# Kernel optimization log

Measured on AMD Instinct MI355X. Metric: run time of the kernel, lower is better.

## Reference

```python
import jax, jax.numpy as jnp
import numpy as np

N_ITER = 30
NMF_EPS = 1e-20
IP_EPS = 1e-20


def nmf_update(Tn, Vn, Yn, eps=NMF_EPS):
    # Tn: (I,K), Vn: (K,J), Yn: (I,J) complex
    Rn = Tn @ Vn
    magR = jnp.abs(Rn)
    YdR = jnp.abs(Yn) ** 2 / (magR ** 2 + eps)   # (I,J)
    Rd = 1.0 / (magR + eps)
    Tn_new = Tn * jnp.sqrt((YdR @ Vn.T) / (Rd @ Vn.T + eps))
    Rn2 = Tn_new @ Vn
    Rd2 = 1.0 / (jnp.abs(Rn2) + eps)
    Vn_new = Vn * jnp.sqrt((Tn_new.T @ YdR) / (Tn_new.T @ Rd2 + eps))
    return Tn_new, Vn_new, Tn_new @ Vn_new


def _ilrma(X, T0, V0):
    M, J, I, _ = X.shape
    N = M
    Xp = jnp.transpose(X, (2, 0, 1, 3))                     # (I,M,J,2)
    X_c = (Xp[..., 0] + 1j * Xp[..., 1]).astype(jnp.complex64)  # (I,M,J)
    eye_M = jnp.eye(M, dtype=jnp.complex64)
    W0 = jnp.tile(eye_M[None], (I, 1, 1))                   # (I,N,M)

    def body(carry, _):
        W, T, V = carry
        Y = jnp.einsum('inm,imj->inj', W, X_c)              # (I,N,J)
        for n in range(N):  # small fixed loop over sources
            Tn, Vn, Rn = nmf_update(T[:, :, n], V[:, :, n], Y[:, n, :])
            T = T.at[:, :, n].set(Tn)
            V = V.at[:, :, n].set(Vn)
            inv_Rn = 1.0 / (Rn + IP_EPS)                    # (I,J) real
            Xw = X_c * jnp.sqrt(inv_Rn)[:, None, :]         # (I,M,J)
            D = jnp.matmul(Xw, jnp.conj(jnp.swapaxes(Xw, 1, 2))) / J  # (I,M,M)
            D_reg = D + IP_EPS * eye_M[None]
            A = jnp.matmul(W, D_reg)                        # (I,N,M)
            e_n = jnp.broadcast_to(eye_M[:, n][None, :, None], (I, M, 1))
            b = jnp.linalg.solve(A, e_n)                    # (I,M,1)
            bH = jnp.conj(jnp.swapaxes(b, 1, 2))
            denom = jnp.matmul(jnp.matmul(bH, D_reg), b).real
            denom = jnp.sqrt(denom + IP_EPS)                # (I,1,1)
            w = jnp.conj((b / denom)[:, :, 0])              # (I,M)
            W = W.at[:, n, :].set(w)
        return (W, T, V), None

    (W, T, V), _ = jax.lax.scan(body, (W0, T0, V0), None, length=N_ITER)
    Y = jnp.einsum('inm,imj->inj', W, X_c)                  # (I,N,J)
    Yo = jnp.transpose(Y, (1, 2, 0))                        # (N,J,I)
    return jnp.stack([Yo.real, Yo.imag], axis=-1)           # (N,J,I,2)


def setup_inputs() -> dict:
    key = jax.random.key(0)
    k1, k2, k3 = jax.random.split(key, 3)
    M, J, I, K = 2, 3000, 2049, 8
    X = jax.random.normal(k1, (M, J, I, 2), dtype=jnp.float32)
    T_init = jax.random.uniform(k2, (I, K, M), dtype=jnp.float32) * (1 - 1e-8) + 1e-8
    V_init = jax.random.uniform(k3, (K, J, M), dtype=jnp.float32) * (1 - 1e-8) + 1e-8
    return {"X": X, "T_init": T_init, "V_init": V_init}


def reference(X, T_init, V_init):
    return _ilrma(X, T_init, V_init)
```

## Files before the change

kernel.cpp:

```cpp
#include <hip/hip_runtime.h>

#define DEVINL __device__ __forceinline__

constexpr int J_ = 3000;
constexpr int I_ = 2049;
constexpr int K_ = 8;
constexpr int NITER = 30;
constexpr float EPS = 1e-20f;
constexpr int JH = 1500;
constexpr int JHP = 1536;
constexpr int JP = 2 * JHP;
constexpr int NL = JHP / 256;
constexpr int TJB = 256;
constexpr int NJTP = JHP / TJB;

typedef float f32x2 __attribute__((ext_vector_type(2)));

DEVINL float waveRed(float v) {
#pragma unroll
  for (int off = 32; off > 0; off >>= 1) v += __shfl_xor(v, off, 64);
  return v;
}

DEVINL float frcp(float x) { return __builtin_amdgcn_rcpf(x); }
DEVINL f32x2 sp(float s) { return (f32x2){s, s}; }
DEVINL f32x2 xy(float4 v) { return (f32x2){v.x, v.y}; }
DEVINL f32x2 zw(float4 v) { return (f32x2){v.z, v.w}; }

__global__ void k_init(const float* __restrict__ Tin, const float* __restrict__ Vin,
                       float* __restrict__ T, float2* __restrict__ V2, float2* __restrict__ W2) {
  int idx = blockIdx.x * 256 + threadIdx.x;
  if (idx < I_ * K_ * 2) {
    int n = idx & 1, rem = idx >> 1;
    int k = rem & 7, i = rem >> 3;
    T[n * I_ * K_ + i * K_ + k] = Tin[idx];
  }
  if (idx < K_ * JP) {
    int k = idx / JP, j = idx - k * JP;
    float2 v = (j < J_) ? ((const float2*)Vin)[k * J_ + j] : make_float2(0.f, 0.f);
    V2[k * JP + j] = v;
  }
  if (idx < I_) {
    W2[idx * 4 + 0] = make_float2(1.f, 0.f);
    W2[idx * 4 + 1] = make_float2(0.f, 0.f);
    W2[idx * 4 + 2] = make_float2(0.f, 0.f);
    W2[idx * 4 + 3] = make_float2(1.f, 0.f);
  }
}

__global__ __launch_bounds__(256) void k_transpose(const float2* __restrict__ X, float2* __restrict__ Xt) {
  __shared__ float2 tile[32][33];
  int m = blockIdx.z;
  int i0 = blockIdx.x * 32, j0 = blockIdx.y * 32;
  int tx = threadIdx.x & 31, ty = threadIdx.x >> 5;
  for (int r = ty; r < 32; r += 8) {
    int j = j0 + r, i = i0 + tx;
    tile[r][tx] = (i < I_ && j < J_) ? X[((size_t)m * J_ + j) * I_ + i] : make_float2(0.f, 0.f);
  }
  __syncthreads();
  for (int r = ty; r < 32; r += 8) {
    int i = i0 + r, j = j0 + tx;
    if (i < I_) Xt[((size_t)m * I_ + i) * JP + j] = tile[tx][r];
  }
}

template <bool DO_C, bool DO_A>
__global__ __launch_bounds__(256, 4) void k_CA(const float4* __restrict__ Xt4,
                                               float2* __restrict__ W2,
                                               float* __restrict__ T,
                                               const float4* __restrict__ V4,
                                               float2* __restrict__ YdR2) {
  const int i = blockIdx.x, t = threadIdx.x;
  const int wave = t >> 6, lane = t & 63;
  f32x2 Tp[K_];
#pragma unroll
  for (int k = 0; k < K_; k++) {
    Tp[k] = (f32x2){T[i * K_ + k], T[I_ * K_ + i * K_ + k]};
  }
  const float4* x0r = Xt4 + (size_t)i * JHP;
  const float4* x1r = Xt4 + (size_t)(I_ + i) * JHP;

  __shared__ f32x2 sR[2][NL][256];
  __shared__ float sred[4][32];
  __shared__ float sout[32];
  __shared__ float sbc[8];

  if constexpr (DO_C) {
    f32x2 an00 = sp(0.f), an11 = sp(0.f), acre = sp(0.f), acim = sp(0.f);
#pragma unroll 2
    for (int l = 0; l < NL; l++) {
      int j2 = t + l * 256;
      float4 x0 = x0r[j2], x1 = x1r[j2];
      f32x2 rA = sp(0.f), rB = sp(0.f);
#pragma unroll
      for (int k = 0; k < K_; k++) {
        float4 vp = V4[(size_t)k * JHP + j2];
        rA += Tp[k] * xy(vp);
        rB += Tp[k] * zw(vp);
      }
      if constexpr (DO_A) {
        sR[0][l][t] = rA;
        sR[1][l][t] = rB;
      }
      f32x2 iA = (f32x2){frcp(rA.x + EPS), frcp(rA.y + EPS)};
      f32x2 iB = (f32x2){frcp(rB.x + EPS), frcp(rB.y + EPS)};
      float n00a = x0.x * x0.x + x0.y * x0.y, n00b = x0.z * x0.z + x0.w * x0.w;
      float n11a = x1.x * x1.x + x1.y * x1.y, n11b = x1.z * x1.z + x1.w * x1.w;
      float crea = x0.x * x1.x + x0.y * x1.y, creb = x0.z * x1.z + x0.w * x1.w;
      float cima = x0.y * x1.x - x0.x * x1.y, cimb = x0.w * x1.z - x0.z * x1.w;
      an00 += sp(n00a) * iA + sp(n00b) * iB;
      an11 += sp(n11a) * iA + sp(n11b) * iB;
      acre += sp(crea) * iA + sp(creb) * iB;
      acim += sp(cima) * iA + sp(cimb) * iB;
    }
    float vals[8] = {an00.x, an11.x, acre.x, acim.x, an00.y, an11.y, acre.y, acim.y};
#pragma unroll
    for (int q = 0; q < 8; q++) {
      float v = waveRed(vals[q]);
      if (lane == 0) sred[wave][q] = v;
    }
    __syncthreads();
    if (t < 8) sout[t] = sred[0][t] + sred[1][t] + sred[2][t] + sred[3][t];
    __syncthreads();
    if (t == 0) {
      const double Jinv = 1.0 / (double)J_;
      double D[2][4];
#pragma unroll
      for (int s2 = 0; s2 < 2; s2++) {
        D[s2][0] = (double)sout[s2 * 4 + 0] * Jinv + (double)EPS;
        D[s2][1] = (double)sout[s2 * 4 + 1] * Jinv + (double)EPS;
        D[s2][2] = (double)sout[s2 * 4 + 2] * Jinv;
        D[s2][3] = (double)sout[s2 * 4 + 3] * Jinv;
      }
      double Wd[2][2][2];
#pragma unroll
      for (int r = 0; r < 2; r++)
#pragma unroll
        for (int c = 0; c < 2; c++) {
          float2 w = W2[i * 4 + r * 2 + c];
          Wd[r][c][0] = w.x;
          Wd[r][c][1] = w.y;
        }
      for (int n2 = 0; n2 < 2; n2++) {
        double d00 = D[n2][0], d11 = D[n2][1], dre = D[n2][2], dim = D[n2][3];
        double A[2][2][2];
#pragma unroll
        for (int r = 0; r < 2; r++) {
          A[r][0][0] = Wd[r][0][0] * d00 + (Wd[r][1][0] * dre + Wd[r][1][1] * dim);
          A[r][0][1] = Wd[r][0][1] * d00 + (Wd[r][1][1] * dre - Wd[r][1][0] * dim);
          A[r][1][0] = Wd[r][1][0] * d11 + (Wd[r][0][0] * dre - Wd[r][0][1] * dim);
          A[r][1][1] = Wd[r][1][1] * d11 + (Wd[r][0][1] * dre + Wd[r][0][0] * dim);
        }
        double detre = A[0][0][0] * A[1][1][0] - A[0][0][1] * A[1][1][1]
                     - (A[0][1][0] * A[1][0][0] - A[0][1][1] * A[1][0][1]);
        double detim = A[0][0][0] * A[1][1][1] + A[0][0][1] * A[1][1][0]
                     - (A[0][1][0] * A[1][0][1] + A[0][1][1] * A[1][0][0]);
        double b0re, b0im, b1re, b1im;
        if (n2 == 0) { b0re = A[1][1][0]; b0im = A[1][1][1]; b1re = -A[1][0][0]; b1im = -A[1][0][1]; }
        else         { b0re = -A[0][1][0]; b0im = -A[0][1][1]; b1re = A[0][0][0]; b1im = A[0][0][1]; }
        double dmag = detre * detre + detim * detim;
        double t0re = (b0re * detre + b0im * detim) / dmag, t0im = (b0im * detre - b0re * detim) / dmag;
        double t1re = (b1re * detre + b1im * detim) / dmag, t1im = (b1im * detre - b1re * detim) / dmag;
        double pre = t0re * t1re + t0im * t1im, pim = t0re * t1im - t0im * t1re;
        double quad = d00 * (t0re * t0re + t0im * t0im) + d11 * (t1re * t1re + t1im * t1im)
                    + 2.0 * (dre * pre - dim * pim);
        double denom = sqrt(quad + (double)EPS);
        double w0re = t0re / denom, w0im = -t0im / denom;
        double w1re = t1re / denom, w1im = -t1im / denom;
        Wd[n2][0][0] = w0re; Wd[n2][0][1] = w0im;
        Wd[n2][1][0] = w1re; Wd[n2][1][1] = w1im;
        W2[i * 4 + n2 * 2 + 0] = make_float2((float)w0re, (float)w0im);
        W2[i * 4 + n2 * 2 + 1] = make_float2((float)w1re, (float)w1im);
      }
      if (DO_A) {
        sbc[0] = (float)(Wd[0][0][0] * Wd[0][0][0] + Wd[0][0][1] * Wd[0][0][1]);
        sbc[1] = (float)(Wd[0][1][0] * Wd[0][1][0] + Wd[0][1][1] * Wd[0][1][1]);
        sbc[2] = (float)(2.0 * (Wd[0][0][0] * Wd[0][1][0] + Wd[0][0][1] * Wd[0][1][1]));
        sbc[3] = (float)(-2.0 * (Wd[0][0][1] * Wd[0][1][0] - Wd[0][0][0] * Wd[0][1][1]));
        sbc[4] = (float)(Wd[1][0][0] * Wd[1][0][0] + Wd[1][0][1] * Wd[1][0][1]);
        sbc[5] = (float)(Wd[1][1][0] * Wd[1][1][0] + Wd[1][1][1] * Wd[1][1][1]);
        sbc[6] = (float)(2.0 * (Wd[1][0][0] * Wd[1][1][0] + Wd[1][0][1] * Wd[1][1][1]));
        sbc[7] = (float)(-2.0 * (Wd[1][0][1] * Wd[1][1][0] - Wd[1][0][0] * Wd[1][1][1]));
      }
    }
  } else {
    if (t == 0) {
      float2 w00 = W2[i * 4 + 0], w01 = W2[i * 4 + 1], w10 = W2[i * 4 + 2], w11 = W2[i * 4 + 3];
      sbc[0] = w00.x * w00.x + w00.y * w00.y;
      sbc[1] = w01.x * w01.x + w01.y * w01.y;
      sbc[2] = 2.f * (w00.x * w01.x + w00.y * w01.y);
      sbc[3] = -2.f * (w00.y * w01.x - w00.x * w01.y);
      sbc[4] = w10.x * w10.x + w10.y * w10.y;
      sbc[5] = w11.x * w11.x + w11.y * w11.y;
      sbc[6] = 2.f * (w10.x * w11.x + w10.y * w11.y);
      sbc[7] = -2.f * (w10.y * w11.x - w10.x * w11.y);
    }
  }

  if constexpr (DO_A) {
    __syncthreads();
    const f32x2 alp = (f32x2){sbc[0], sbc[4]}, btp = (f32x2){sbc[1], sbc[5]};
    const f32x2 gmp = (f32x2){sbc[2], sbc[6]}, dlp = (f32x2){sbc[3], sbc[7]};
    f32x2 nT[K_], dT[K_];
#pragma unroll
    for (int k = 0; k < K_; k++) { nT[k] = sp(0.f); dT[k] = sp(0.f); }
    float2* y0r = YdR2 + (size_t)i * JHP;
    float2* y1r = YdR2 + (size_t)(I_ + i) * JHP;
#pragma unroll 1
    for (int l = 0; l < NL; l++) {
      int j2 = t + l * 256;
      float4 x0 = x0r[j2], x1 = x1r[j2];
      f32x2 rA, rB;
      if constexpr (DO_C) {
        rA = sR[0][l][t];
        rB = sR[1][l][t];
      } else {
        rA = sp(0.f); rB = sp(0.f);
#pragma unroll
        for (int k = 0; k < K_; k++) {
          float4 vp = V4[(size_t)k * JHP + j2];
          rA += Tp[k] * xy(vp);
          rB += Tp[k] * zw(vp);
        }
      }
      float n00a = x0.x * x0.x + x0.y * x0.y, n00b = x0.z * x0.z + x0.w * x0.w;
      float n11a = x1.x * x1.x + x1.y * x1.y, n11b = x1.z * x1.z + x1.w * x1.w;
      float crea = x0.x * x1.x + x0.y * x1.y, creb = x0.z * x1.z + x0.w * x1.w;
      float cima = x0.y * x1.x - x0.x * x1.y, cimb = x0.w * x1.z - x0.z * x1.w;
      f32x2 aA = alp * n00a + btp * n11a + gmp * crea + dlp * cima;
      f32x2 aB = alp * n00b + btp * n11b + gmp * creb + dlp * cimb;
      f32x2 ydrA = aA * (f32x2){frcp(rA.x * rA.x + EPS), frcp(rA.y * rA.y + EPS)};
      f32x2 ydrB = aB * (f32x2){frcp(rB.x * rB.x + EPS), frcp(rB.y * rB.y + EPS)};
      f32x2 rdA = (f32x2){frcp(rA.x + EPS), frcp(rA.y + EPS)};
      f32x2 rdB = (f32x2){frcp(rB.x + EPS), frcp(rB.y + EPS)};
      y0r[j2] = make_float2(ydrA.x, ydrB.x);
      y1r[j2] = make_float2(ydrA.y, ydrB.y);
#pragma unroll
      for (int k = 0; k < K_; k++) {
        float4 vp = V4[(size_t)k * JHP + j2];
        nT[k] += ydrA * xy(vp) + ydrB * zw(vp);
        dT[k] += rdA * xy(vp) + rdB * zw(vp);
      }
    }
#pragma unroll
    for (int k = 0; k < K_; k++) {
      float a = waveRed(nT[k].x); if (lane == 0) sred[wave][k] = a;
      float b = waveRed(dT[k].x); if (lane == 0) sred[wave][8 + k] = b;
      float c = waveRed(nT[k].y); if (lane == 0) sred[wave][16 + k] = c;
      float d = waveRed(dT[k].y); if (lane == 0) sred[wave][24 + k] = d;
    }
    __syncthreads();
    if (t < 32) sout[t] = sred[0][t] + sred[1][t] + sred[2][t] + sred[3][t];
    __syncthreads();
    if (t < 16) {
      int n = t >> 3, k = t & 7;
      float num = sout[n * 16 + k];
      float den = sout[n * 16 + 8 + k];
      float told = T[n * I_ * K_ + i * K_ + k];
      T[n * I_ * K_ + i * K_ + k] = told * sqrtf(num / (den + EPS));
    }
  }
}

__global__ __launch_bounds__(TJB, 4) void k_passB(const float* __restrict__ T,
                                                  const float4* __restrict__ V4,
                                                  const float2* __restrict__ YdR2,
                                                  float2* __restrict__ partial2, int iseg) {
  int t = threadIdx.x;
  int jt = blockIdx.x, s = blockIdx.y, n = blockIdx.z;
  int j2 = jt * TJB + t;
  f32x2 va2[K_];
#pragma unroll
  for (int k = 0; k < K_; k++) {
    float4 vp = V4[(size_t)k * JHP + j2];
    va2[k] = (n == 0) ? (f32x2){vp.x, vp.z} : (f32x2){vp.y, vp.w};
  }
  int i0 = s * iseg, i1 = min(i0 + iseg, I_);
  const float2* yb = YdR2 + (size_t)n * I_ * JHP;
  const float* Tb = T + (size_t)n * I_ * K_;
  f32x2 nV[K_], dV[K_];
#pragma unroll
  for (int k = 0; k < K_; k++) { nV[k] = sp(0.f); dV[k] = sp(0.f); }
#pragma unroll 4
  for (int i = i0; i < i1; i++) {
    const float4* tp = (const float4*)(Tb + i * K_);
    float4 t03 = tp[0], t47 = tp[1];
    float Tn[K_] = {t03.x, t03.y, t03.z, t03.w, t47.x, t47.y, t47.z, t47.w};
    float2 yl = yb[(size_t)i * JHP + j2];
    f32x2 y = (f32x2){yl.x, yl.y};
    f32x2 R = sp(0.f);
#pragma unroll
    for (int k = 0; k < K_; k++) R += sp(Tn[k]) * va2[k];
    f32x2 rd = (f32x2){frcp(R.x + EPS), frcp(R.y + EPS)};
#pragma unroll
    for (int k = 0; k < K_; k++) {
      nV[k] += sp(Tn[k]) * y;
      dV[k] += sp(Tn[k]) * rd;
    }
  }
  if (j2 < JH) {
    size_t b0 = (size_t)((s * 2 + n) * 2 + 0) * K_ * JH;
    size_t b1 = (size_t)((s * 2 + n) * 2 + 1) * K_ * JH;
#pragma unroll
    for (int k = 0; k < K_; k++) {
      partial2[b0 + (size_t)k * JH + j2] = make_float2(nV[k].x, nV[k].y);
      partial2[b1 + (size_t)k * JH + j2] = make_float2(dV[k].x, dV[k].y);
    }
  }
}

__global__ void k_finV(const float* __restrict__ partial, float* __restrict__ Vf, int nseg) {
  int idx = blockIdx.x * 256 + threadIdx.x;
  if (idx >= 2 * K_ * J_) return;
  int n = idx / (K_ * J_);
  int rem = idx - n * (K_ * J_);
  int k = rem / J_, j = rem - k * J_;
  float num = 0.f, den = 0.f;
  for (int s = 0; s < nseg; s++) {
    num += partial[((size_t)((s * 2 + n) * 2 + 0) * K_ + k) * J_ + j];
    den += partial[((size_t)((s * 2 + n) * 2 + 1) * K_ + k) * J_ + j];
  }
  float res = sqrtf(num / (den + EPS));
  Vf[((size_t)k * JP + j) * 2 + n] *= res;
}

__global__ __launch_bounds__(256) void k_output(const float2* __restrict__ Xt,
                                                const float2* __restrict__ W2,
                                                float2* __restrict__ out) {
  __shared__ float2 tile[2][32][33];
  int i0 = blockIdx.x * 32, j0 = blockIdx.y * 32;
  int tx = threadIdx.x & 31, ty = threadIdx.x >> 5;
  for (int r = ty; r < 32; r += 8) {
    int i = i0 + r, j = j0 + tx;
    if (i < I_ && j < J_) {
      float2 w00 = W2[i * 4 + 0], w01 = W2[i * 4 + 1], w10 = W2[i * 4 + 2], w11 = W2[i * 4 + 3];
      float2 x0 = Xt[(size_t)i * JP + j], x1 = Xt[((size_t)I_ + i) * JP + j];
      tile[0][r][tx] = make_float2(w00.x * x0.x - w00.y * x0.y + w01.x * x1.x - w01.y * x1.y,
                                   w00.x * x0.y + w00.y * x0.x + w01.x * x1.y + w01.y * x1.x);
      tile[1][r][tx] = make_float2(w10.x * x0.x - w10.y * x0.y + w11.x * x1.x - w11.y * x1.y,
                                   w10.x * x0.y + w10.y * x0.x + w11.x * x1.y + w11.y * x1.x);
    }
  }
  __syncthreads();
  for (int r = ty; r < 32; r += 8) {
    int j = j0 + r, i = i0 + tx;
    if (i < I_ && j < J_) {
      out[((size_t)0 * J_ + j) * I_ + i] = tile[0][tx][r];
      out[((size_t)1 * J_ + j) * I_ + i] = tile[1][tx][r];
    }
  }
}

extern "C" void kernel_launch(void* const* d_in, const int* in_sizes, int n_in,
                              void* d_out, int out_size, void* d_ws, size_t ws_size,
                              hipStream_t stream) {
  const float* X = (const float*)d_in[0];
  const float* Tin = (const float*)d_in[1];
  const float* Vin = (const float*)d_in[2];

  char* ws = (char*)d_ws;
  size_t off = 0;
  auto alloc = [&](size_t bytes) {
    void* p = ws + off;
    off = (off + bytes + 255) & ~(size_t)255;
    return p;
  };
  float2* Xt = (float2*)alloc((size_t)2 * I_ * JP * sizeof(float2));
  float2* YdR2 = (float2*)alloc((size_t)2 * I_ * JHP * sizeof(float2));
  float2* V2 = (float2*)alloc((size_t)K_ * JP * sizeof(float2));
  float* T = (float*)alloc((size_t)2 * I_ * K_ * sizeof(float));
  float2* W2 = (float2*)alloc((size_t)I_ * 4 * sizeof(float2));
  size_t per_seg = (size_t)2 * 2 * K_ * J_ * sizeof(float);
  int nseg = (off + 64 * per_seg <= ws_size) ? 64 : ((off + 32 * per_seg <= ws_size) ? 32 : 16);
  float* partial = (float*)alloc((size_t)nseg * per_seg);
  int iseg = (I_ + nseg - 1) / nseg;
  (void)in_sizes; (void)n_in; (void)out_size;

  const float4* Xt4 = (const float4*)Xt;
  const float4* V4 = (const float4*)V2;

  k_init<<<(I_ * K_ * 2 + 255) / 256, 256, 0, stream>>>(Tin, Vin, T, V2, W2);
  dim3 tg((I_ + 31) / 32, JP / 32, 2);
  k_transpose<<<tg, 256, 0, stream>>>((const float2*)X, Xt);

  k_CA<false, true><<<I_, 256, 0, stream>>>(Xt4, W2, T, V4, YdR2);
  for (int it = 0; it < NITER; it++) {
    k_passB<<<dim3(NJTP, nseg, 2), TJB, 0, stream>>>(T, V4, YdR2, (float2*)partial, iseg);
    k_finV<<<(2 * K_ * J_ + 255) / 256, 256, 0, stream>>>(partial, (float*)V2, nseg);
    if (it < NITER - 1) {
      k_CA<true, true><<<I_, 256, 0, stream>>>(Xt4, W2, T, V4, YdR2);
    } else {
      k_CA<true, false><<<I_, 256, 0, stream>>>(Xt4, W2, T, V4, YdR2);
    }
  }
  dim3 og((I_ + 31) / 32, (J_ + 31) / 32);
  k_output<<<og, 256, 0, stream>>>(Xt, W2, (float2*)d_out);
}
```

Before: 3.196 ms.

## Process two frequency rows per block in k_CA to share V loads

Each k_CA block now handles rows i and i+1025, so the grid shrinks to 1025 blocks. In the covariance pass the V tile loaded per j is reused for both rows' model reconstructions. The IP solve is factored into a helper run by two threads, and the T-update pass loops over both rows. Shared memory for sR doubles and register pressure rises, which may reduce occupancy. The second pass still reloads V separately for each row.

```diff
diff --git a/kernel.cpp b/kernel.cpp
--- a/kernel.cpp
+++ b/kernel.cpp
@@ -13,6 +13,7 @@
 constexpr int NL = JHP / 256;
 constexpr int TJB = 256;
 constexpr int NJTP = JHP / TJB;
+constexpr int IBLK = 1025;
 
 typedef float f32x2 __attribute__((ext_vector_type(2)));
 
@@ -64,200 +65,243 @@
   }
 }
 
+DEVINL void ip_solve(const float* sout8, float2* W2, int irow, float* sbc8, bool fill_sbc) {
+  const double Jinv = 1.0 / (double)J_;
+  double D[2][4];
+#pragma unroll
+  for (int s2 = 0; s2 < 2; s2++) {
+    D[s2][0] = (double)sout8[s2 * 4 + 0] * Jinv + (double)EPS;
+    D[s2][1] = (double)sout8[s2 * 4 + 1] * Jinv + (double)EPS;
+    D[s2][2] = (double)sout8[s2 * 4 + 2] * Jinv;
+    D[s2][3] = (double)sout8[s2 * 4 + 3] * Jinv;
+  }
+  double Wd[2][2][2];
+#pragma unroll
+  for (int r = 0; r < 2; r++)
+#pragma unroll
+    for (int c = 0; c < 2; c++) {
+      float2 w = W2[irow * 4 + r * 2 + c];
+      Wd[r][c][0] = w.x;
+      Wd[r][c][1] = w.y;
+    }
+  for (int n2 = 0; n2 < 2; n2++) {
+    double d00 = D[n2][0], d11 = D[n2][1], dre = D[n2][2], dim = D[n2][3];
+    double A[2][2][2];
+#pragma unroll
+    for (int r = 0; r < 2; r++) {
+      A[r][0][0] = Wd[r][0][0] * d00 + (Wd[r][1][0] * dre + Wd[r][1][1] * dim);
+      A[r][0][1] = Wd[r][0][1] * d00 + (Wd[r][1][1] * dre - Wd[r][1][0] * dim);
+      A[r][1][0] = Wd[r][1][0] * d11 + (Wd[r][0][0] * dre - Wd[r][0][1] * dim);
+      A[r][1][1] = Wd[r][1][1] * d11 + (Wd[r][0][1] * dre + Wd[r][0][0] * dim);
+    }
+    double detre = A[0][0][0] * A[1][1][0] - A[0][0][1] * A[1][1][1]
+                 - (A[0][1][0] * A[1][0][0] - A[0][1][1] * A[1][0][1]);
+    double detim = A[0][0][0] * A[1][1][1] + A[0][0][1] * A[1][1][0]
+                 - (A[0][1][0] * A[1][0][1] + A[0][1][1] * A[1][0][0]);
+    double b0re, b0im, b1re, b1im;
+    if (n2 == 0) { b0re = A[1][1][0]; b0im = A[1][1][1]; b1re = -A[1][0][0]; b1im = -A[1][0][1]; }
+    else         { b0re = -A[0][1][0]; b0im = -A[0][1][1]; b1re = A[0][0][0]; b1im = A[0][0][1]; }
+    double dmag = detre * detre + detim * detim;
+    double t0re = (b0re * detre + b0im * detim) / dmag, t0im = (b0im * detre - b0re * detim) / dmag;
+    double t1re = (b1re * detre + b1im * detim) / dmag, t1im = (b1im * detre - b1re * detim) / dmag;
+    double pre = t0re * t1re + t0im * t1im, pim = t0re * t1im - t0im * t1re;
+    double quad = d00 * (t0re * t0re + t0im * t0im) + d11 * (t1re * t1re + t1im * t1im)
+                + 2.0 * (dre * pre - dim * pim);
+    double denom = sqrt(quad + (double)EPS);
+    double w0re = t0re / denom, w0im = -t0im / denom;
+    double w1re = t1re / denom, w1im = -t1im / denom;
+    Wd[n2][0][0] = w0re; Wd[n2][0][1] = w0im;
+    Wd[n2][1][0] = w1re; Wd[n2][1][1] = w1im;
+    W2[irow * 4 + n2 * 2 + 0] = make_float2((float)w0re, (float)w0im);
+    W2[irow * 4 + n2 * 2 + 1] = make_float2((float)w1re, (float)w1im);
+  }
+  if (fill_sbc) {
+    sbc8[0] = (float)(Wd[0][0][0] * Wd[0][0][0] + Wd[0][0][1] * Wd[0][0][1]);
+    sbc8[1] = (float)(Wd[0][1][0] * Wd[0][1][0] + Wd[0][1][1] * Wd[0][1][1]);
+    sbc8[2] = (float)(2.0 * (Wd[0][0][0] * Wd[0][1][0] + Wd[0][0][1] * Wd[0][1][1]));
+    sbc8[3] = (float)(-2.0 * (Wd[0][0][1] * Wd[0][1][0] - Wd[0][0][0] * Wd[0][1][1]));
+    sbc8[4] = (float)(Wd[1][0][0] * Wd[1][0][0] + Wd[1][0][1] * Wd[1][0][1]);
+    sbc8[5] = (float)(Wd[1][1][0] * Wd[1][1][0] + Wd[1][1][1] * Wd[1][1][1]);
+    sbc8[6] = (float)(2.0 * (Wd[1][0][0] * Wd[1][1][0] + Wd[1][0][1] * Wd[1][1][1]));
+    sbc8[7] = (float)(-2.0 * (Wd[1][0][1] * Wd[1][1][0] - Wd[1][0][0] * Wd[1][1][1]));
+  }
+}
+
 template <bool DO_C, bool DO_A>
 __global__ __launch_bounds__(256, 4) void k_CA(const float4* __restrict__ Xt4,
                                                float2* __restrict__ W2,
                                                float* __restrict__ T,
                                                const float4* __restrict__ V4,
                                                float2* __restrict__ YdR2) {
-  const int i = blockIdx.x, t = threadIdx.x;
+  const int t = threadIdx.x;
   const int wave = t >> 6, lane = t & 63;
-  f32x2 Tp[K_];
+  const int i0 = blockIdx.x;
+  const int i1raw = blockIdx.x + IBLK;
+  const bool act1 = (i1raw < I_);
+  const int i1 = act1 ? i1raw : i0;
+
+  f32x2 Tp0[K_], Tp1[K_];
 #pragma unroll
   for (int k = 0; k < K_; k++) {
-    Tp[k] = (f32x2){T[i * K_ + k], T[I_ * K_ + i * K_ + k]};
-  }
-  const float4* x0r = Xt4 + (size_t)i * JHP;
-  const float4* x1r = Xt4 + (size_t)(I_ + i) * JHP;
-
-  __shared__ f32x2 sR[2][NL][256];
+    Tp0[k] = (f32x2){T[i0 * K_ + k], T[I_ * K_ + i0 * K_ + k]};
+    Tp1[k] = (f32x2){T[i1 * K_ + k], T[I_ * K_ + i1 * K_ + k]};
+  }
+
+  __shared__ f32x2 sR[2][2][NL][256];
   __shared__ float sred[4][32];
-  __shared__ float sout[32];
-  __shared__ float sbc[8];
+  __shared__ float soutC[2][8];
+  __shared__ float soutA[32];
+  __shared__ float sbc[2][8];
 
   if constexpr (DO_C) {
-    f32x2 an00 = sp(0.f), an11 = sp(0.f), acre = sp(0.f), acim = sp(0.f);
-#pragma unroll 2
-    for (int l = 0; l < NL; l++) {
-      int j2 = t + l * 256;
-      float4 x0 = x0r[j2], x1 = x1r[j2];
-      f32x2 rA = sp(0.f), rB = sp(0.f);
-#pragma unroll
-      for (int k = 0; k < K_; k++) {
-        float4 vp = V4[(size_t)k * JHP + j2];
-        rA += Tp[k] * xy(vp);
-        rB += Tp[k] * zw(vp);
-      }
-      if constexpr (DO_A) {
-        sR[0][l][t] = rA;
-        sR[1][l][t] = rB;
-      }
-      f32x2 iA = (f32x2){frcp(rA.x + EPS), frcp(rA.y + EPS)};
-      f32x2 iB = (f32x2){frcp(rB.x + EPS), frcp(rB.y + EPS)};
-      float n00a = x0.x * x0.x + x0.y * x0.y, n00b = x0.z * x0.z + x0.w * x0.w;
-      float n11a = x1.x * x1.x + x1.y * x1.y, n11b = x1.z * x1.z + x1.w * x1.w;
-      float crea = x0.x * x1.x + x0.y * x1.y, creb = x0.z * x1.z + x0.w * x1.w;
-      float cima = x0.y * x1.x - x0.x * x1.y, cimb = x0.w * x1.z - x0.z * x1.w;
-      an00 += sp(n00a) * iA + sp(n00b) * iB;
-      an11 += sp(n11a) * iA + sp(n11b) * iB;
-      acre += sp(crea) * iA + sp(creb) * iB;
-      acim += sp(cima) * iA + sp(cimb) * iB;
-    }
-    float vals[8] = {an00.x, an11.x, acre.x, acim.x, an00.y, an11.y, acre.y, acim.y};
-#pragma unroll
-    for (int q = 0; q < 8; q++) {
-      float v = waveRed(vals[q]);
-      if (lane == 0) sred[wave][q] = v;
-    }
-    __syncthreads();
-    if (t < 8) sout[t] = sred[0][t] + sred[1][t] + sred[2][t] + sred[3][t];
-    __syncthreads();
-    if (t == 0) {
-      const double Jinv = 1.0 / (double)J_;
-      double D[2][4];
-#pragma unroll
-      for (int s2 = 0; s2 < 2; s2++) {
-        D[s2][0] = (double)sout[s2 * 4 + 0] * Jinv + (double)EPS;
-        D[s2][1] = (double)sout[s2 * 4 + 1] * Jinv + (double)EPS;
-        D[s2][2] = (double)sout[s2 * 4 + 2] * Jinv;
-        D[s2][3] = (double)sout[s2 * 4 + 3] * Jinv;
-      }
-      double Wd[2][2][2];
-#pragma unroll
-      for (int r = 0; r < 2; r++)
-#pragma unroll
-        for (int c = 0; c < 2; c++) {
-          float2 w = W2[i * 4 + r * 2 + c];
-          Wd[r][c][0] = w.x;
-          Wd[r][c][1] = w.y;
-        }
-      for (int n2 = 0; n2 < 2; n2++) {
-        double d00 = D[n2][0], d11 = D[n2][1], dre = D[n2][2], dim = D[n2][3];
-        double A[2][2][2];
-#pragma unroll
-        for (int r = 0; r < 2; r++) {
-          A[r][0][0] = Wd[r][0][0] * d00 + (Wd[r][1][0] * dre + Wd[r][1][1] * dim);
-          A[r][0][1] = Wd[r][0][1] * d00 + (Wd[r][1][1] * dre - Wd[r][1][0] * dim);
-          A[r][1][0] = Wd[r][1][0] * d11 + (Wd[r][0][0] * dre - Wd[r][0][1] * dim);
-          A[r][1][1] = Wd[r][1][1] * d11 + (Wd[r][0][1] * dre + Wd[r][0][0] * dim);
-        }
-        double detre = A[0][0][0] * A[1][1][0] - A[0][0][1] * A[1][1][1]
-                     - (A[0][1][0] * A[1][0][0] - A[0][1][1] * A[1][0][1]);
-        double detim = A[0][0][0] * A[1][1][1] + A[0][0][1] * A[1][1][0]
-                     - (A[0][1][0] * A[1][0][1] + A[0][1][1] * A[1][0][0]);
-        double b0re, b0im, b1re, b1im;
-        if (n2 == 0) { b0re = A[1][1][0]; b0im = A[1][1][1]; b1re = -A[1][0][0]; b1im = -A[1][0][1]; }
-        else         { b0re = -A[0][1][0]; b0im = -A[0][1][1]; b1re = A[0][0][0]; b1im = A[0][0][1]; }
-        double dmag = detre * detre + detim * detim;
-        double t0re = (b0re * detre + b0im * detim) / dmag, t0im = (b0im * detre - b0re * detim) / dmag;
-        double t1re = (b1re * detre + b1im * detim) / dmag, t1im = (b1im * detre - b1re * detim) / dmag;
-        double pre = t0re * t1re + t0im * t1im, pim = t0re * t1im - t0im * t1re;
-        double quad = d00 * (t0re * t0re + t0im * t0im) + d11 * (t1re * t1re + t1im * t1im)
-                    + 2.0 * (dre * pre - dim * pim);
-        double denom = sqrt(quad + (double)EPS);
-        double w0re = t0re / denom, w0im = -t0im / denom;
-        double w1re = t1re / denom, w1im = -t1im / denom;
-        Wd[n2][0][0] = w0re; Wd[n2][0][1] = w0im;
-        Wd[n2][1][0] = w1re; Wd[n2][1][1] = w1im;
-        W2[i * 4 + n2 * 2 + 0] = make_float2((float)w0re, (float)w0im);
-        W2[i * 4 + n2 * 2 + 1] = make_float2((float)w1re, (float)w1im);
-      }
-      if (DO_A) {
-        sbc[0] = (float)(Wd[0][0][0] * Wd[0][0][0] + Wd[0][0][1] * Wd[0][0][1]);
-        sbc[1] = (float)(Wd[0][1][0] * Wd[0][1][0] + Wd[0][1][1] * Wd[0][1][1]);
-        sbc[2] = (float)(2.0 * (Wd[0][0][0] * Wd[0][1][0] + Wd[0][0][1] * Wd[0][1][1]));
-        sbc[3] = (float)(-2.0 * (Wd[0][0][1] * Wd[0][1][0] - Wd[0][0][0] * Wd[0][1][1]));
-        sbc[4] = (float)(Wd[1][0][0] * Wd[1][0][0] + Wd[1][0][1] * Wd[1][0][1]);
-        sbc[5] = (float)(Wd[1][1][0] * Wd[1][1][0] + Wd[1][1][1] * Wd[1][1][1]);
-        sbc[6] = (float)(2.0 * (Wd[1][0][0] * Wd[1][1][0] + Wd[1][0][1] * Wd[1][1][1]));
-        sbc[7] = (float)(-2.0 * (Wd[1][0][1] * Wd[1][1][0] - Wd[1][0][0] * Wd[1][1][1]));
-      }
-    }
-  } else {
-    if (t == 0) {
-      float2 w00 = W2[i * 4 + 0], w01 = W2[i * 4 + 1], w10 = W2[i * 4 + 2], w11 = W2[i * 4 + 3];
-      sbc[0] = w00.x * w00.x + w00.y * w00.y;
-      sbc[1] = w01.x * w01.x + w01.y * w01.y;
-      sbc[2] = 2.f * (w00.x * w01.x + w00.y * w01.y);
-      sbc[3] = -2.f * (w00.y * w01.x - w00.x * w01.y);
-      sbc[4] = w10.x * w10.x + w10.y * w10.y;
-      sbc[5] = w11.x * w11.x + w11.y * w11.y;
-      sbc[6] = 2.f * (w10.x * w11.x + w10.y * w11.y);
-      sbc[7] = -2.f * (w10.y * w11.x - w10.x * w11.y);
-    }
-  }
-
-  if constexpr (DO_A) {
-    __syncthreads();
-    const f32x2 alp = (f32x2){sbc[0], sbc[4]}, btp = (f32x2){sbc[1], sbc[5]};
-    const f32x2 gmp = (f32x2){sbc[2], sbc[6]}, dlp = (f32x2){sbc[3], sbc[7]};
-    f32x2 nT[K_], dT[K_];
-#pragma unroll
-    for (int k = 0; k < K_; k++) { nT[k] = sp(0.f); dT[k] = sp(0.f); }
-    float2* y0r = YdR2 + (size_t)i * JHP;
-    float2* y1r = YdR2 + (size_t)(I_ + i) * JHP;
+    const float4* x0r0 = Xt4 + (size_t)i0 * JHP;
+    const float4* x1r0 = Xt4 + (size_t)(I_ + i0) * JHP;
+    const float4* x0r1 = Xt4 + (size_t)i1 * JHP;
+    const float4* x1r1 = Xt4 + (size_t)(I_ + i1) * JHP;
+    f32x2 an00_0 = sp(0.f), an11_0 = sp(0.f), acre_0 = sp(0.f), acim_0 = sp(0.f);
+    f32x2 an00_1 = sp(0.f), an11_1 = sp(0.f), acre_1 = sp(0.f), acim_1 = sp(0.f);
 #pragma unroll 1
     for (int l = 0; l < NL; l++) {
       int j2 = t + l * 256;
-      float4 x0 = x0r[j2], x1 = x1r[j2];
-      f32x2 rA, rB;
-      if constexpr (DO_C) {
-        rA = sR[0][l][t];
-        rB = sR[1][l][t];
-      } else {
-        rA = sp(0.f); rB = sp(0.f);
+      float4 x0a = x0r0[j2], x1a = x1r0[j2];
+      float4 x0b = x0r1[j2], x1b = x1r1[j2];
+      f32x2 rA0 = sp(0.f), rB0 = sp(0.f), rA1 = sp(0.f), rB1 = sp(0.f);
+#pragma unroll
+      for (int k = 0; k < K_; k++) {
+        float4 vp = V4[(size_t)k * JHP + j2];
+        rA0 += Tp0[k] * xy(vp); rB0 += Tp0[k] * zw(vp);
+        rA1 += Tp1[k] * xy(vp); rB1 += Tp1[k] * zw(vp);
+      }
+      if constexpr (DO_A) {
+        sR[0][0][l][t] = rA0; sR[0][1][l][t] = rB0;
+        sR[1][0][l][t] = rA1; sR[1][1][l][t] = rB1;
+      }
+      {
+        f32x2 iA = (f32x2){frcp(rA0.x + EPS), frcp(rA0.y + EPS)};
+        f32x2 iB = (f32x2){frcp(rB0.x + EPS), frcp(rB0.y + EPS)};
+        float n00a = x0a.x * x0a.x + x0a.y * x0a.y, n00b = x0a.z * x0a.z + x0a.w * x0a.w;
+        float n11a = x1a.x * x1a.x + x1a.y * x1a.y, n11b = x1a.z * x1a.z + x1a.w * x1a.w;
+        float crea = x0a.x * x1a.x + x0a.y * x1a.y, creb = x0a.z * x1a.z + x0a.w * x1a.w;
+        float cima = x0a.y * x1a.x - x0a.x * x1a.y, cimb = x0a.w * x1a.z - x0a.z * x1a.w;
+        an00_0 += sp(n00a) * iA + sp(n00b) * iB;
+        an11_0 += sp(n11a) * iA + sp(n11b) * iB;
+        acre_0 += sp(crea) * iA + sp(creb) * iB;
+        acim_0 += sp(cima) * iA + sp(cimb) * iB;
+      }
+      {
+        f32x2 iA = (f32x2){frcp(rA1.x + EPS), frcp(rA1.y + EPS)};
+        f32x2 iB = (f32x2){frcp(rB1.x + EPS), frcp(rB1.y + EPS)};
+        float n00a = x0b.x * x0b.x + x0b.y * x0b.y, n00b = x0b.z * x0b.z + x0b.w * x0b.w;
+        float n11a = x1b.x * x1b.x + x1b.y * x1b.y, n11b = x1b.z * x1b.z + x1b.w * x1b.w;
+        float crea = x0b.x * x1b.x + x0b.y * x1b.y, creb = x0b.z * x1b.z + x0b.w * x1b.w;
+        float cima = x0b.y * x1b.x - x0b.x * x1b.y, cimb = x0b.w * x1b.z - x0b.z * x1b.w;
+        an00_1 += sp(n00a) * iA + sp(n00b) * iB;
+        an11_1 += sp(n11a) * iA + sp(n11b) * iB;
+        acre_1 += sp(crea) * iA + sp(creb) * iB;
+        acim_1 += sp(cima) * iA + sp(cimb) * iB;
+      }
+    }
+    float vals[16] = {an00_0.x, an11_0.x, acre_0.x, acim_0.x, an00_0.y, an11_0.y, acre_0.y, acim_0.y,
+                      an00_1.x, an11_1.x, acre_1.x, acim_1.x, an00_1.y, an11_1.y, acre_1.y, acim_1.y};
+#pragma unroll
+    for (int q = 0; q < 16; q++) {
+      float v = waveRed(vals[q]);
+      if (lane == 0) sred[wave][q] = v;
+    }
+    __syncthreads();
+    if (t < 16) {
+      int r = t >> 3, q = t & 7;
+      soutC[r][q] = sred[0][t] + sred[1][t] + sred[2][t] + sred[3][t];
+    }
+    __syncthreads();
+    if (t == 0) ip_solve(soutC[0], W2, i0, sbc[0], DO_A);
+    if (t == 64 && act1) ip_solve(soutC[1], W2, i1, sbc[1], DO_A);
+  } else {
+    if (t == 0 || (t == 64 && act1)) {
+      int r = t >> 6;
+      int irow = r ? i1 : i0;
+      float2 w00 = W2[irow * 4 + 0], w01 = W2[irow * 4 + 1], w10 = W2[irow * 4 + 2], w11 = W2[irow * 4 + 3];
+      sbc[r][0] = w00.x * w00.x + w00.y * w00.y;
+      sbc[r][1] = w01.x * w01.x + w01.y * w01.y;
+      sbc[r][2] = 2.f * (w00.x * w01.x + w00.y * w01.y);
+      sbc[r][3] = -2.f * (w00.y * w01.x - w00.x * w01.y);
+      sbc[r][4] = w10.x * w10.x + w10.y * w10.y;
+      sbc[r][5] = w11.x * w11.x + w11.y * w11.y;
+      sbc[r][6] = 2.f * (w10.x * w11.x + w10.y * w11.y);
+      sbc[r][7] = -2.f * (w10.y * w11.x - w10.x * w11.y);
+    }
+  }
+
+  if constexpr (DO_A) {
+    __syncthreads();
+#pragma unroll
+    for (int r = 0; r < 2; r++) {
+      const bool act = (r == 0) || act1;
+      const int irow = r ? i1 : i0;
+      const f32x2 alp = (f32x2){sbc[r][0], sbc[r][4]}, btp = (f32x2){sbc[r][1], sbc[r][5]};
+      const f32x2 gmp = (f32x2){sbc[r][2], sbc[r][6]}, dlp = (f32x2){sbc[r][3], sbc[r][7]};
+      const float4* xr0 = Xt4 + (size_t)irow * JHP;
+      const float4* xr1 = Xt4 + (size_t)(I_ + irow) * JHP;
+      float2* y0r = YdR2 + (size_t)irow * JHP;
+      float2* y1r = YdR2 + (size_t)(I_ + irow) * JHP;
+      f32x2 nT[K_], dT[K_];
+#pragma unroll
+      for (int k = 0; k < K_; k++) { nT[k] = sp(0.f); dT[k] = sp(0.f); }
+#pragma unroll 1
+      for (int l = 0; l < NL; l++) {
+        int j2 = t + l * 256;
+        float4 x0 = xr0[j2], x1 = xr1[j2];
+        f32x2 rA, rB;
+        if constexpr (DO_C) {
+          rA = sR[r][0][l][t];
+          rB = sR[r][1][l][t];
+        } else {
+          rA = sp(0.f); rB = sp(0.f);
+#pragma unroll
+          for (int k = 0; k < K_; k++) {
+            float4 vp = V4[(size_t)k * JHP + j2];
+            if (r == 0) { rA += Tp0[k] * xy(vp); rB += Tp0[k] * zw(vp); }
+            else        { rA += Tp1[k] * xy(vp); rB += Tp1[k] * zw(vp); }
+          }
+        }
+        float n00a = x0.x * x0.x + x0.y * x0.y, n00b = x0.z * x0.z + x0.w * x0.w;
+        float n11a = x1.x * x1.x + x1.y * x1.y, n11b = x1.z * x1.z + x1.w * x1.w;
+        float crea = x0.x * x1.x + x0.y * x1.y, creb = x0.z * x1.z + x0.w * x1.w;
+        float cima = x0.y * x1.x - x0.x * x1.y, cimb = x0.w * x1.z - x0.z * x1.w;
+        f32x2 aA = alp * n00a + btp * n11a + gmp * crea + dlp * cima;
+        f32x2 aB = alp * n00b + btp * n11b + gmp * creb + dlp * cimb;
+        f32x2 ydrA = aA * (f32x2){frcp(rA.x * rA.x + EPS), frcp(rA.y * rA.y + EPS)};
+        f32x2 ydrB = aB * (f32x2){frcp(rB.x * rB.x + EPS), frcp(rB.y * rB.y + EPS)};
+        f32x2 rdA = (f32x2){frcp(rA.x + EPS), frcp(rA.y + EPS)};
+        f32x2 rdB = (f32x2){frcp(rB.x + EPS), frcp(rB.y + EPS)};
+        if (act) {
+          y0r[j2] = make_float2(ydrA.x, ydrB.x);
+          y1r[j2] = make_float2(ydrA.y, ydrB.y);
+        }
 #pragma unroll
         for (int k = 0; k < K_; k++) {
           float4 vp = V4[(size_t)k * JHP + j2];
-          rA += Tp[k] * xy(vp);
-          rB += Tp[k] * zw(vp);
+          nT[k] += ydrA * xy(vp) + ydrB * zw(vp);
+          dT[k] += rdA * xy(vp) + rdB * zw(vp);
         }
       }
-      float n00a = x0.x * x0.x + x0.y * x0.y, n00b = x0.z * x0.z + x0.w * x0.w;
-      float n11a = x1.x * x1.x + x1.y * x1.y, n11b = x1.z * x1.z + x1.w * x1.w;
-      float crea = x0.x * x1.x + x0.y * x1.y, creb = x0.z * x1.z + x0.w * x1.w;
-      float cima = x0.y * x1.x - x0.x * x1.y, cimb = x0.w * x1.z - x0.z * x1.w;
-      f32x2 aA = alp * n00a + btp * n11a + gmp * crea + dlp * cima;
-      f32x2 aB = alp * n00b + btp * n11b + gmp * creb + dlp * cimb;
-      f32x2 ydrA = aA * (f32x2){frcp(rA.x * rA.x + EPS), frcp(rA.y * rA.y + EPS)};
-      f32x2 ydrB = aB * (f32x2){frcp(rB.x * rB.x + EPS), frcp(rB.y * rB.y + EPS)};
-      f32x2 rdA = (f32x2){frcp(rA.x + EPS), frcp(rA.y + EPS)};
-      f32x2 rdB = (f32x2){frcp(rB.x + EPS), frcp(rB.y + EPS)};
-      y0r[j2] = make_float2(ydrA.x, ydrB.x);
-      y1r[j2] = make_float2(ydrA.y, ydrB.y);
 #pragma unroll
       for (int k = 0; k < K_; k++) {
-        float4 vp = V4[(size_t)k * JHP + j2];
-        nT[k] += ydrA * xy(vp) + ydrB * zw(vp);
-        dT[k] += rdA * xy(vp) + rdB * zw(vp);
-      }
-    }
-#pragma unroll
-    for (int k = 0; k < K_; k++) {
-      float a = waveRed(nT[k].x); if (lane == 0) sred[wave][k] = a;
-      float b = waveRed(dT[k].x); if (lane == 0) sred[wave][8 + k] = b;
-      float c = waveRed(nT[k].y); if (lane == 0) sred[wave][16 + k] = c;
-      float d = waveRed(dT[k].y); if (lane == 0) sred[wave][24 + k] = d;
-    }
-    __syncthreads();
-    if (t < 32) sout[t] = sred[0][t] + sred[1][t] + sred[2][t] + sred[3][t];
-    __syncthreads();
-    if (t < 16) {
-      int n = t >> 3, k = t & 7;
-      float num = sout[n * 16 + k];
-      float den = sout[n * 16 + 8 + k];
-      float told = T[n * I_ * K_ + i * K_ + k];
-      T[n * I_ * K_ + i * K_ + k] = told * sqrtf(num / (den + EPS));
+        float a = waveRed(nT[k].x); if (lane == 0) sred[wave][k] = a;
+        float b = waveRed(dT[k].x); if (lane == 0) sred[wave][8 + k] = b;
+        float c = waveRed(nT[k].y); if (lane == 0) sred[wave][16 + k] = c;
+        float d = waveRed(dT[k].y); if (lane == 0) sred[wave][24 + k] = d;
+      }
+      __syncthreads();
+      if (t < 32) soutA[t] = sred[0][t] + sred[1][t] + sred[2][t] + sred[3][t];
+      __syncthreads();
+      if (t < 16 && act) {
+        int n = t >> 3, k = t & 7;
+        float num = soutA[n * 16 + k];
+        float den = soutA[n * 16 + 8 + k];
+        float told = T[n * I_ * K_ + irow * K_ + k];
+        T[n * I_ * K_ + irow * K_ + k] = told * sqrtf(num / (den + EPS));
+      }
     }
   }
 }
@@ -383,14 +427,14 @@
   dim3 tg((I_ + 31) / 32, JP / 32, 2);
   k_transpose<<<tg, 256, 0, stream>>>((const float2*)X, Xt);
 
-  k_CA<false, true><<<I_, 256, 0, stream>>>(Xt4, W2, T, V4, YdR2);
+  k_CA<false, true><<<IBLK, 256, 0, stream>>>(Xt4, W2, T, V4, YdR2);
   for (int it = 0; it < NITER; it++) {
     k_passB<<<dim3(NJTP, nseg, 2), TJB, 0, stream>>>(T, V4, YdR2, (float2*)partial, iseg);
     k_finV<<<(2 * K_ * J_ + 255) / 256, 256, 0, stream>>>(partial, (float*)V2, nseg);
     if (it < NITER - 1) {
-      k_CA<true, true><<<I_, 256, 0, stream>>>(Xt4, W2, T, V4, YdR2);
+      k_CA<true, true><<<IBLK, 256, 0, stream>>>(Xt4, W2, T, V4, YdR2);
     } else {
-      k_CA<true, false><<<I_, 256, 0, stream>>>(Xt4, W2, T, V4, YdR2);
+      k_CA<true, false><<<IBLK, 256, 0, stream>>>(Xt4, W2, T, V4, YdR2);
     }
   }
   dim3 og((I_ + 31) / 32, (J_ + 31) / 32);
```

Result: slower. 3.373 ms (+5.5%).
